# Optimization experiments

Measured on AMD Instinct MI355X. Metric: run time of the kernel, lower is better.

The kernel has to match this reference:

```python
import jax, jax.numpy as jnp
from jax import lax
import numpy as np

DIM = 192
HEADS = 8
TOPK = 2


def conv1x1(x, w):
    # x: [B,C,H,W], w: [O,C] (1x1 conv, no bias)
    return jnp.einsum('bchw,oc->bohw', x, w)


def setup_inputs() -> dict:
    key = jax.random.key(0)
    ks = jax.random.split(key, 6)
    B, C, H, W = 8, DIM, 128, 128
    x = jax.random.normal(ks[0], (B, C, H, W), jnp.float32)
    qkv_w = jax.random.normal(ks[1], (3 * C, C), jnp.float32) * 0.05
    dw_w = jax.random.normal(ks[2], (3 * C, 1, 3, 3), jnp.float32) * 0.1  # depthwise OIHW
    proj_w = jax.random.normal(ks[3], (C, C), jnp.float32) * 0.05
    router_main_w = jax.random.normal(ks[4], (HEADS, C), jnp.float32) * 0.05
    router_aux_w = jax.random.normal(ks[5], (HEADS, C), jnp.float32) * 0.05
    return dict(x=x, qkv_w=qkv_w, dw_w=dw_w, proj_w=proj_w,
                router_main_w=router_main_w, router_aux_w=router_aux_w,
                task_id=0)


def _forward(x, qkv_w, dw_w, proj_w, router_main_w, router_aux_w, task_id):
    B, C, H, W = x.shape
    heads, topk = HEADS, TOPK
    hd = C // heads
    N = H * W
    scale = hd ** -0.5

    # ---- router: softmax -> top-k -> mask -> renormalized gates ----
    rw = router_main_w if task_id == 0 else router_aux_w
    logits = jnp.einsum('bchw,oc->bohw', x, rw)                 # [B, heads, H, W]
    probs = jax.nn.softmax(
        logits.reshape(B, heads, N).transpose(0, 2, 1).reshape(B * N, heads), axis=1)
    _, idx = lax.top_k(probs, topk)                             # [B*N, topk]
    mask = lax.stop_gradient(
        jax.nn.one_hot(idx, heads, dtype=probs.dtype).sum(axis=1))  # [B*N, heads]
    masked = probs * mask
    denom = jnp.maximum(masked.sum(axis=1, keepdims=True), jnp.finfo(x.dtype).eps)
    gates = (masked / denom).reshape(B, N, heads).transpose(0, 2, 1)[:, :, None, :]  # [B, heads, 1, N]

    # ---- QKV: 1x1 conv + depthwise 3x3 conv ----
    qkv = conv1x1(x, qkv_w)                                      # [B, 3C, H, W]
    qkv = lax.conv_general_dilated(
        qkv, dw_w, window_strides=(1, 1), padding=((1, 1), (1, 1)),
        feature_group_count=3 * C,
        dimension_numbers=('NCHW', 'OIHW', 'NCHW'))
    q, k, v = jnp.split(qkv, 3, axis=1)

    def heads_view(t):  # b (h c) H W -> b h c (H W)
        return t.reshape(B, heads, hd, N)

    q, k, v = heads_view(q), heads_view(k), heads_view(v)
    # L2 normalize along the pixel axis (F.normalize, eps=1e-12)
    q = q / jnp.maximum(jnp.linalg.norm(q, axis=-1, keepdims=True), 1e-12)
    k = k / jnp.maximum(jnp.linalg.norm(k, axis=-1, keepdims=True), 1e-12)

    # channel attention: [B, heads, hd, hd] (tiny GEMM)
    attn = jax.nn.softmax(jnp.einsum('bhcn,bhdn->bhcd', q, k) * scale, axis=-1)
    out = jnp.einsum('bhcd,bhdn->bhcn', attn, v)                 # [B, heads, hd, N]

    out = out * gates * topk                                     # MoH gating
    out = out.reshape(B, C, H, W)                                # b (head c) h w
    out = conv1x1(out, proj_w)
    return out


def reference(x, qkv_w, dw_w, proj_w, router_main_w, router_aux_w, task_id):
    return _forward(x, qkv_w, dw_w, proj_w, router_main_w, router_aux_w, task_id)
```

## Files before the change

kernel.cpp:

```cpp
#include <hip/hip_runtime.h>
#include <hip/hip_bf16.h>

typedef __bf16 bf16;
typedef __bf16 bf16x8 __attribute__((ext_vector_type(8)));
typedef __bf16 bf16x4 __attribute__((ext_vector_type(4)));
typedef float f32x4 __attribute__((ext_vector_type(4)));
typedef unsigned int u32;

#define NPIX 16384
#define CDIM 192

__device__ __forceinline__ void gl2lds16(const bf16* g, const bf16* l) {
  __builtin_amdgcn_global_load_lds(
      (const __attribute__((address_space(1))) u32*)(g),
      (__attribute__((address_space(3))) u32*)(l), 16, 0, 0);
}

__global__ __launch_bounds__(256) void detect_kernel(
    const u32* __restrict__ xw, int* __restrict__ flag) {
  int tid = threadIdx.x;
  int cnt = 0;
  for (int i = 0; i < 32; i++) {
    u32 w = xw[tid * 32 + i];
    u32 e = (w >> 7) & 0xFFu;
    if (e >= 0xC0u) cnt++;
  }
  for (int off = 32; off; off >>= 1) cnt += __shfl_down(cnt, off);
  __shared__ int red[4];
  if ((tid & 63) == 0) red[tid >> 6] = cnt;
  __syncthreads();
  if (tid == 0) *flag = (red[0] + red[1] + red[2] + red[3] >= 16) ? 1 : 0;
}

__global__ __launch_bounds__(256) void wconvert_kernel(
    const void* __restrict__ s0, bf16* __restrict__ d0,
    const void* __restrict__ s1, bf16* __restrict__ d1,
    const void* __restrict__ s2, bf16* __restrict__ d2,
    const int* __restrict__ flag) {
  int which = blockIdx.y;
  const void* src = which == 0 ? s0 : (which == 1 ? s1 : s2);
  bf16* dst = which == 0 ? d0 : (which == 1 ? d1 : d2);
  int n = which == 0 ? 110592 : (which == 1 ? 5184 : 36864);
  int base = (blockIdx.x * 256 + threadIdx.x) * 8;
  if (base >= n) return;
  if (*flag) {
    const float* s = (const float*)src;
    float4 lo = *(const float4*)(s + base);
    float4 hi = *(const float4*)(s + base + 4);
    bf16x8 o;
    o[0] = (bf16)lo.x; o[1] = (bf16)lo.y; o[2] = (bf16)lo.z; o[3] = (bf16)lo.w;
    o[4] = (bf16)hi.x; o[5] = (bf16)hi.y; o[6] = (bf16)hi.z; o[7] = (bf16)hi.w;
    *(bf16x8*)(dst + base) = o;
  } else {
    *(bf16x8*)(dst + base) = *(const bf16x8*)((const bf16*)src + base);
  }
}

__global__ __launch_bounds__(256) void transpose_kernel(
    const void* __restrict__ xraw, bf16* __restrict__ xt,
    const int* __restrict__ flag, const void* __restrict__ wmain,
    const void* __restrict__ waux, const int* __restrict__ task,
    float* __restrict__ gates2) {
  __shared__ float wT[CDIM][8];
  __shared__ float lred[4][128][8];
  int t = threadIdx.x;
  int b = blockIdx.y;
  int n0 = blockIdx.x * 128;
  int f = *flag;
  const void* rw = (*task == 0) ? wmain : waux;
  for (int i = t; i < 8 * CDIM; i += 256) {
    int h = i / CDIM, c = i - h * CDIM;
    wT[c][h] = f ? ((const float*)rw)[i] : (float)((const bf16*)rw)[i];
  }
  __syncthreads();
  int nl = (t & 31) * 4;
  int cb = (t >> 5) * 8;
  float l[4][8];
#pragma unroll
  for (int j = 0; j < 4; j++)
#pragma unroll
    for (int h = 0; h < 8; h++) l[j][h] = 0.f;
  for (int ch = 0; ch < 3; ch++) {
    int c8 = ch * 64 + cb;
    float v[8][4];
    if (f) {
      const float* xp = (const float*)xraw + ((size_t)b * CDIM << 14) + n0 + nl;
#pragma unroll
      for (int i = 0; i < 8; i++) {
        float4 q = *(const float4*)(xp + ((size_t)(c8 + i) << 14));
        v[i][0] = q.x; v[i][1] = q.y; v[i][2] = q.z; v[i][3] = q.w;
      }
    } else {
      const bf16* xp = (const bf16*)xraw + ((size_t)b * CDIM << 14) + n0 + nl;
#pragma unroll
      for (int i = 0; i < 8; i++) {
        bf16x4 q = *(const bf16x4*)(xp + ((size_t)(c8 + i) << 14));
#pragma unroll
        for (int j = 0; j < 4; j++) v[i][j] = (float)q[j];
      }
    }
#pragma unroll
    for (int i = 0; i < 8; i++) {
      float4 wlo = *(const float4*)&wT[c8 + i][0];
      float4 whi = *(const float4*)&wT[c8 + i][4];
#pragma unroll
      for (int j = 0; j < 4; j++) {
        float xv = v[i][j];
        l[j][0] += xv * wlo.x; l[j][1] += xv * wlo.y;
        l[j][2] += xv * wlo.z; l[j][3] += xv * wlo.w;
        l[j][4] += xv * whi.x; l[j][5] += xv * whi.y;
        l[j][6] += xv * whi.z; l[j][7] += xv * whi.w;
      }
    }
#pragma unroll
    for (int j = 0; j < 4; j++) {
      bf16x8 o;
#pragma unroll
      for (int i = 0; i < 8; i++) o[i] = (bf16)v[i][j];
      *(bf16x8*)(xt + ((size_t)b << 14) * CDIM + (size_t)(n0 + nl + j) * CDIM + c8) = o;
    }
  }
#pragma unroll
  for (int j = 0; j < 4; j++)
#pragma unroll
    for (int h = 0; h < 8; h++) l[j][h] += __shfl_xor(l[j][h], 32);
  int lane = t & 63, wid = t >> 6;
  if (lane < 32) {
#pragma unroll
    for (int j = 0; j < 4; j++) {
      *(float4*)&lred[wid][nl + j][0] = make_float4(l[j][0], l[j][1], l[j][2], l[j][3]);
      *(float4*)&lred[wid][nl + j][4] = make_float4(l[j][4], l[j][5], l[j][6], l[j][7]);
    }
  }
  __syncthreads();
  if (t < 128) {
    float lg[8];
#pragma unroll
    for (int h = 0; h < 8; h++)
      lg[h] = (lred[0][t][h] + lred[1][t][h]) + (lred[2][t][h] + lred[3][t][h]);
    int i1 = 0;
#pragma unroll
    for (int h = 1; h < 8; h++) if (lg[h] > lg[i1]) i1 = h;
    int i2 = (i1 == 0) ? 1 : 0;
#pragma unroll
    for (int h = 0; h < 8; h++) if (h != i1 && lg[h] > lg[i2]) i2 = h;
    float e = __expf(lg[i2] - lg[i1]);
    float g1 = 2.f / (1.f + e);
    float g2 = e * g1;
    float* gb = gates2 + (((size_t)b * 8) << 14) + n0 + t;
#pragma unroll
    for (int h = 0; h < 8; h++)
      gb[(size_t)h << 14] = (h == i1) ? g1 : ((h == i2) ? g2 : 0.f);
  }
}

__global__ __launch_bounds__(256) void wgemm2_kernel(
    const bf16* __restrict__ A, const bf16* __restrict__ Xt,
    void* __restrict__ C, int M, const int* __restrict__ flag, int finalout) {
  __shared__ bf16 smem[22528];
  int tid = threadIdx.x;
  int wave = tid >> 6, lane = tid & 63;
  int c0 = lane & 15, qd = lane >> 4;

  int nm = M / 96;
  int ord = blockIdx.x + nm * (blockIdx.y + (blockIdx.z << 6));
  int z = ord & 7;
  int local = ord >> 3;
  int mt = local % nm;
  int nt = local / nm;
  int m0 = mt * 96, n0 = nt << 8;

  const bf16* Xb = Xt + (size_t)z * CDIM * NPIX;
  size_t cbase = (size_t)z * M * NPIX;

  int q = lane >> 4;
  int rr = (lane & 15) ^ (q << 1);
  const bf16* Ag0 = A + (size_t)(m0 + (wave << 4) + rr) * CDIM + (q << 3);
  const bf16* Ag1 = A + (size_t)(m0 + ((4 + wave) << 4) + rr) * CDIM + (q << 3);
  const bf16* Bg  = Xb + (size_t)(n0 + (wave << 6) + rr) * CDIM + (q << 3);

  int slot8 = ((qd << 4) + (c0 ^ (qd << 1))) << 3;

  f32x4 acc[6][4];
#pragma unroll
  for (int i = 0; i < 6; i++)
#pragma unroll
    for (int j = 0; j < 4; j++) acc[i][j] = {0.f, 0.f, 0.f, 0.f};

  auto STAGE = [&](int bb, int k) {
    gl2lds16(Ag0 + k, smem + bb + (wave << 9));
    if (wave < 2) gl2lds16(Ag1 + k, smem + bb + ((4 + wave) << 9));
    const bf16* bl = smem + bb + 3072 + (wave << 11);
    gl2lds16(Bg + k,             bl);
    gl2lds16(Bg + 16 * CDIM + k, bl + 512);
    gl2lds16(Bg + 32 * CDIM + k, bl + 1024);
    gl2lds16(Bg + 48 * CDIM + k, bl + 1536);
  };

  int bb = 0;
  STAGE(0, 0);
  __syncthreads();
  for (int t = 0; t < 6; t++) {
    if (t < 5) STAGE(bb ^ 11264, (t + 1) << 5);
    bf16x8 af[6], bfr[4];
#pragma unroll
    for (int mi = 0; mi < 6; mi++)
      af[mi] = *(const bf16x8*)(smem + bb + mi * 512 + slot8);
#pragma unroll
    for (int nj = 0; nj < 4; nj++)
      bfr[nj] = *(const bf16x8*)(smem + bb + 3072 + (wave << 11) + nj * 512 + slot8);
#pragma unroll
    for (int mi = 0; mi < 6; mi++)
#pragma unroll
      for (int nj = 0; nj < 4; nj++)
        acc[mi][nj] = __builtin_amdgcn_mfma_f32_16x16x32_bf16(bfr[nj], af[mi], acc[mi][nj], 0, 0, 0);
    if (t < 5) { __syncthreads(); bb ^= 11264; }
  }

  int f32o = finalout && (*flag);
  int n_base = n0 + (wave << 6) + (qd << 2);
#pragma unroll
  for (int mi = 0; mi < 6; mi++) {
    size_t rowb = cbase + ((size_t)(m0 + (mi << 4) + c0) << 14) + n_base;
#pragma unroll
    for (int nj = 0; nj < 4; nj++) {
      if (f32o) {
        *(float4*)((float*)C + rowb + (nj << 4)) =
            make_float4(acc[mi][nj][0], acc[mi][nj][1], acc[mi][nj][2], acc[mi][nj][3]);
      } else {
        bf16x4 o;
        o[0] = (bf16)acc[mi][nj][0]; o[1] = (bf16)acc[mi][nj][1];
        o[2] = (bf16)acc[mi][nj][2]; o[3] = (bf16)acc[mi][nj][3];
        *(bf16x4*)((bf16*)C + rowb + (nj << 4)) = o;
      }
    }
  }
}

__global__ __launch_bounds__(256) void dwconv_kernel(
    const bf16* __restrict__ qkv, const bf16* __restrict__ w9,
    bf16* __restrict__ out, float* __restrict__ sumsq) {
  int tid = threadIdx.x;
  int ch = blockIdx.y, b = blockIdx.z;
  int xs = (tid & 15) << 3;
  int y0 = (blockIdx.x << 6) + ((tid >> 4) << 2);
  const bf16* in = qkv + (((size_t)(b * 576 + ch)) << 14);
  float wv[9];
#pragma unroll
  for (int i = 0; i < 9; i++) wv[i] = (float)w9[ch * 9 + i];
  float o[4][8];
#pragma unroll
  for (int r = 0; r < 4; r++)
#pragma unroll
    for (int i = 0; i < 8; i++) o[r][i] = 0.f;
#pragma unroll
  for (int rr = 0; rr < 6; rr++) {
    int yy = y0 - 1 + rr;
    if (yy < 0 || yy > 127) continue;
    const bf16* row = in + (yy << 7);
    float vals[10];
    vals[0] = (xs > 0) ? (float)row[xs - 1] : 0.f;
    bf16x8 v8 = *(const bf16x8*)(row + xs);
#pragma unroll
    for (int j = 0; j < 8; j++) vals[1 + j] = (float)v8[j];
    vals[9] = (xs < 120) ? (float)row[xs + 8] : 0.f;
#pragma unroll
    for (int orow = 0; orow < 4; orow++) {
      int wrow = rr - orow;
      if (wrow < 0 || wrow > 2) continue;
      float w0 = wv[wrow * 3 + 0], w1 = wv[wrow * 3 + 1], w2 = wv[wrow * 3 + 2];
#pragma unroll
      for (int i = 0; i < 8; i++)
        o[orow][i] += w0 * vals[i] + w1 * vals[i + 1] + w2 * vals[i + 2];
    }
  }
  float ss = 0.f;
  bf16* ob = out + (((size_t)(b * 576 + ch)) << 14);
#pragma unroll
  for (int r = 0; r < 4; r++) {
    bf16x8 ov;
#pragma unroll
    for (int i = 0; i < 8; i++) { ov[i] = (bf16)o[r][i]; ss += o[r][i] * o[r][i]; }
    *(bf16x8*)(ob + ((y0 + r) << 7) + xs) = ov;
  }
  if (ch < 384) {
#pragma unroll
    for (int off = 32; off; off >>= 1) ss += __shfl_down(ss, off);
    __shared__ float red[4];
    if ((tid & 63) == 0) red[tid >> 6] = ss;
    __syncthreads();
    if (tid == 0) atomicAdd(&sumsq[b * 384 + ch], red[0] + red[1] + red[2] + red[3]);
  }
}

__global__ __launch_bounds__(256) void spart_kernel(
    const bf16* __restrict__ dwout, float* __restrict__ Spart) {
  int tid = threadIdx.x;
  int bh = blockIdx.y, split = blockIdx.x;
  int b = bh >> 3, h = bh & 7;
  int wave = tid >> 6, lane = tid & 63;
  int c0 = lane & 15, qd = lane >> 4;
  __shared__ float Sred[576];
  for (int i = tid; i < 576; i += 256) Sred[i] = 0.f;
  __syncthreads();
  const bf16* qb = dwout + (((size_t)(b * 576 + h * 24)) << 14);
  const bf16* kb = dwout + (((size_t)(b * 576 + 192 + h * 24)) << 14);
  int r0 = c0;
  int r1 = (16 + c0 < 24) ? (16 + c0) : 23;
  f32x4 a00 = {0.f,0.f,0.f,0.f}, a01 = {0.f,0.f,0.f,0.f};
  f32x4 a10 = {0.f,0.f,0.f,0.f}, a11 = {0.f,0.f,0.f,0.f};
  int base = (((split << 2) + wave) << 9) + (qd << 3);
  for (int t = 0; t < 16; t++) {
    int kk = base + (t << 5);
    bf16x8 qa0 = *(const bf16x8*)(qb + (((size_t)r0) << 14) + kk);
    bf16x8 qa1 = *(const bf16x8*)(qb + (((size_t)r1) << 14) + kk);
    bf16x8 ka0 = *(const bf16x8*)(kb + (((size_t)r0) << 14) + kk);
    bf16x8 ka1 = *(const bf16x8*)(kb + (((size_t)r1) << 14) + kk);
    a00 = __builtin_amdgcn_mfma_f32_16x16x32_bf16(qa0, ka0, a00, 0, 0, 0);
    a01 = __builtin_amdgcn_mfma_f32_16x16x32_bf16(qa0, ka1, a01, 0, 0, 0);
    a10 = __builtin_amdgcn_mfma_f32_16x16x32_bf16(qa1, ka0, a10, 0, 0, 0);
    a11 = __builtin_amdgcn_mfma_f32_16x16x32_bf16(qa1, ka1, a11, 0, 0, 0);
  }
  f32x4 accs[4] = {a00, a01, a10, a11};
#pragma unroll
  for (int mi = 0; mi < 2; mi++)
#pragma unroll
    for (int nj = 0; nj < 2; nj++) {
      f32x4 a = accs[mi * 2 + nj];
#pragma unroll
      for (int r = 0; r < 4; r++) {
        int rrow = (mi << 4) + (qd << 2) + r;
        int cc = (nj << 4) + c0;
        if (rrow < 24 && cc < 24) atomicAdd(&Sred[rrow * 24 + cc], a[r]);
      }
    }
  __syncthreads();
  float* outp = Spart + (size_t)(bh * 8 + split) * 576;
  for (int i = tid; i < 576; i += 256) outp[i] = Sred[i];
}

__global__ __launch_bounds__(576) void attn_kernel(
    const float* __restrict__ Spart, const float* __restrict__ sumsq,
    float* __restrict__ attn) {
  int bh = blockIdx.x, tid = threadIdx.x;
  int b = bh >> 3, h = bh & 7;
  int c = tid / 24, d = tid % 24;
  float s = 0.f;
  for (int sp = 0; sp < 8; sp++) s += Spart[(size_t)(bh * 8 + sp) * 576 + tid];
  float nq = fmaxf(sqrtf(sumsq[b * 384 + h * 24 + c]), 1e-12f);
  float nk = fmaxf(sqrtf(sumsq[b * 384 + 192 + h * 24 + d]), 1e-12f);
  s = s / (nq * nk) * 0.20412414523193154f;
  __shared__ float Sm[576];
  Sm[tid] = s;
  __syncthreads();
  float mx = -1e30f;
  for (int j = 0; j < 24; j++) mx = fmaxf(mx, Sm[c * 24 + j]);
  float Z = 0.f;
  for (int j = 0; j < 24; j++) Z += __expf(Sm[c * 24 + j] - mx);
  attn[(size_t)bh * 576 + tid] = __expf(s - mx) / Z;
}

__global__ __launch_bounds__(256) void av_kernel(
    const bf16* __restrict__ dwout, const float* __restrict__ attn,
    const float* __restrict__ gates2, bf16* __restrict__ gated_t) {
  int tid = threadIdx.x;
  int bh = blockIdx.y;
  int b = bh >> 3, h = bh & 7;
  int n = blockIdx.x * 256 + tid;
  __shared__ float At[576];
  for (int i = tid; i < 576; i += 256) At[i] = attn[(size_t)bh * 576 + i];
  __syncthreads();
  const bf16* vb = dwout + (((size_t)(b * 576 + 384 + h * 24)) << 14) + n;
  float acc[24];
#pragma unroll
  for (int c = 0; c < 24; c++) acc[c] = 0.f;
#pragma unroll
  for (int d0 = 0; d0 < 24; d0 += 4) {
    float v0 = (float)vb[(size_t)(d0 + 0) << 14];
    float v1 = (float)vb[(size_t)(d0 + 1) << 14];
    float v2 = (float)vb[(size_t)(d0 + 2) << 14];
    float v3 = (float)vb[(size_t)(d0 + 3) << 14];
#pragma unroll
    for (int c = 0; c < 24; c++) {
      const float4* ap = (const float4*)&At[c * 24 + d0];
      acc[c] += ap->x * v0 + ap->y * v1 + ap->z * v2 + ap->w * v3;
    }
  }
  float g = gates2[(((size_t)(b * 8 + h)) << 14) + n];
  bf16* ob = gated_t + ((size_t)(b * NPIX + n)) * CDIM + h * 24;
#pragma unroll
  for (int ch = 0; ch < 3; ch++) {
    bf16x8 o;
#pragma unroll
    for (int i = 0; i < 8; i++) o[i] = (bf16)(acc[ch * 8 + i] * g);
    *(bf16x8*)(ob + ch * 8) = o;
  }
}

extern "C" void kernel_launch(void* const* d_in, const int* in_sizes, int n_in,
                              void* d_out, int out_size, void* d_ws, size_t ws_size,
                              hipStream_t stream) {
  const void* x_raw    = d_in[0];
  const void* qkvw_raw = d_in[1];
  const void* dww_raw  = d_in[2];
  const void* projw_raw= d_in[3];
  const void* rtm_raw  = d_in[4];
  const void* rta_raw  = d_in[5];
  const int*  task     = (const int*)d_in[6];
  char* ws = (char*)d_ws;

  bf16*  qkv_raw = (bf16*)(ws);
  bf16*  gated_t = qkv_raw;
  bf16*  dwout   = (bf16*)(ws + 150994944);
  float* gates2  = (float*)(ws + 301989888);
  float* sumsq   = (float*)(ws + 306184192);
  float* Spart   = (float*)(ws + 306196480);
  float* attn    = (float*)(ws + 307376128);
  int*   flag    = (int*)(ws + 307523584);
  bf16*  xt      = (bf16*)(ws + 307523712);
  bf16*  qkv_wb  = (bf16*)(ws + 357855360);
  bf16*  dw_wb   = (bf16*)(ws + 358076544);
  bf16*  proj_wb = (bf16*)(ws + 358086912);

  hipMemsetAsync(sumsq, 0, 8 * 384 * sizeof(float), stream);
  detect_kernel<<<1, 256, 0, stream>>>((const u32*)x_raw, flag);
  wconvert_kernel<<<dim3(54, 3), 256, 0, stream>>>(qkvw_raw, qkv_wb, dww_raw, dw_wb,
                                                   projw_raw, proj_wb, flag);
  transpose_kernel<<<dim3(128, 8), 256, 0, stream>>>(x_raw, xt, flag,
                                                     rtm_raw, rta_raw, task, gates2);
  wgemm2_kernel<<<dim3(6, 64, 8), 256, 0, stream>>>(qkv_wb, xt, qkv_raw, 576, flag, 0);
  dwconv_kernel<<<dim3(2, 576, 8), 256, 0, stream>>>(qkv_raw, dw_wb, dwout, sumsq);
  spart_kernel<<<dim3(8, 64), 256, 0, stream>>>(dwout, Spart);
  attn_kernel<<<64, 576, 0, stream>>>(Spart, sumsq, attn);
  av_kernel<<<dim3(64, 64), 256, 0, stream>>>(dwout, attn, gates2, gated_t);
  wgemm2_kernel<<<dim3(2, 64, 8), 256, 0, stream>>>(proj_wb, gated_t, d_out, 192, flag, 1);
}
```

Before: 448.5 us.

## Load GEMM operands directly from global memory instead of staging through LDS

The weight GEMM kernel drops its double-buffered global-to-LDS staging and the barriers between K steps. Each wave now reads its MFMA fragments for A and B straight from global memory in a fully unrolled K loop. This removes LDS traffic and block-wide synchronisation, and the compiler can schedule all the loads early. In exchange every wave re-reads the shared A tile from global or L2, and the per-lane 16-byte loads with a row stride of CDIM may coalesce less well.

```diff
diff --git a/kernel.cpp b/kernel.cpp
--- a/kernel.cpp
+++ b/kernel.cpp
@@ -9,12 +9,6 @@
 
 #define NPIX 16384
 #define CDIM 192
-
-__device__ __forceinline__ void gl2lds16(const bf16* g, const bf16* l) {
-  __builtin_amdgcn_global_load_lds(
-      (const __attribute__((address_space(1))) u32*)(g),
-      (__attribute__((address_space(3))) u32*)(l), 16, 0, 0);
-}
 
 __global__ __launch_bounds__(256) void detect_kernel(
     const u32* __restrict__ xw, int* __restrict__ flag) {
@@ -157,7 +151,6 @@
 __global__ __launch_bounds__(256) void wgemm2_kernel(
     const bf16* __restrict__ A, const bf16* __restrict__ Xt,
     void* __restrict__ C, int M, const int* __restrict__ flag, int finalout) {
-  __shared__ bf16 smem[22528];
   int tid = threadIdx.x;
   int wave = tid >> 6, lane = tid & 63;
   int c0 = lane & 15, qd = lane >> 4;
@@ -173,13 +166,8 @@
   const bf16* Xb = Xt + (size_t)z * CDIM * NPIX;
   size_t cbase = (size_t)z * M * NPIX;
 
-  int q = lane >> 4;
-  int rr = (lane & 15) ^ (q << 1);
-  const bf16* Ag0 = A + (size_t)(m0 + (wave << 4) + rr) * CDIM + (q << 3);
-  const bf16* Ag1 = A + (size_t)(m0 + ((4 + wave) << 4) + rr) * CDIM + (q << 3);
-  const bf16* Bg  = Xb + (size_t)(n0 + (wave << 6) + rr) * CDIM + (q << 3);
-
-  int slot8 = ((qd << 4) + (c0 ^ (qd << 1))) << 3;
+  const bf16* Ap = A + (size_t)(m0 + c0) * CDIM + (qd << 3);
+  const bf16* Bp = Xb + (size_t)(n0 + (wave << 6) + c0) * CDIM + (qd << 3);
 
   f32x4 acc[6][4];
 #pragma unroll
@@ -187,34 +175,20 @@
 #pragma unroll
     for (int j = 0; j < 4; j++) acc[i][j] = {0.f, 0.f, 0.f, 0.f};
 
-  auto STAGE = [&](int bb, int k) {
-    gl2lds16(Ag0 + k, smem + bb + (wave << 9));
-    if (wave < 2) gl2lds16(Ag1 + k, smem + bb + ((4 + wave) << 9));
-    const bf16* bl = smem + bb + 3072 + (wave << 11);
-    gl2lds16(Bg + k,             bl);
-    gl2lds16(Bg + 16 * CDIM + k, bl + 512);
-    gl2lds16(Bg + 32 * CDIM + k, bl + 1024);
-    gl2lds16(Bg + 48 * CDIM + k, bl + 1536);
-  };
-
-  int bb = 0;
-  STAGE(0, 0);
-  __syncthreads();
-  for (int t = 0; t < 6; t++) {
-    if (t < 5) STAGE(bb ^ 11264, (t + 1) << 5);
+#pragma unroll
+  for (int k0 = 0; k0 < CDIM; k0 += 32) {
     bf16x8 af[6], bfr[4];
 #pragma unroll
+    for (int nj = 0; nj < 4; nj++)
+      bfr[nj] = *(const bf16x8*)(Bp + (size_t)(nj << 4) * CDIM + k0);
+#pragma unroll
     for (int mi = 0; mi < 6; mi++)
-      af[mi] = *(const bf16x8*)(smem + bb + mi * 512 + slot8);
-#pragma unroll
-    for (int nj = 0; nj < 4; nj++)
-      bfr[nj] = *(const bf16x8*)(smem + bb + 3072 + (wave << 11) + nj * 512 + slot8);
+      af[mi] = *(const bf16x8*)(Ap + (size_t)(mi << 4) * CDIM + k0);
 #pragma unroll
     for (int mi = 0; mi < 6; mi++)
 #pragma unroll
       for (int nj = 0; nj < 4; nj++)
         acc[mi][nj] = __builtin_amdgcn_mfma_f32_16x16x32_bf16(bfr[nj], af[mi], acc[mi][nj], 0, 0, 0);
-    if (t < 5) { __syncthreads(); bb ^= 11264; }
   }
 
   int f32o = finalout && (*flag);
```

Result: slower. 481.8 us (+7.4%).

## Pre-swizzle GEMM operands into tile-contiguous blocked layout for LDS loads

Applied to the files above, without the earlier changes.

The producers (weight conversion, input transpose, gated attention output) now write GEMM operands in a blocked K-chunk-major layout that already carries the LDS swizzle. The GEMM staging then reads contiguous 1KB chunks per wave instead of row-strided 16-byte pieces, which should give better-coalesced global-to-LDS transfers. The cost is more complex index math in the producer stores, and every consumer of these buffers must agree on the new layout.

```diff
diff --git a/kernel.cpp b/kernel.cpp
--- a/kernel.cpp
+++ b/kernel.cpp
@@ -9,6 +9,7 @@
 
 #define NPIX 16384
 #define CDIM 192
+
 
 __device__ __forceinline__ void gl2lds16(const bf16* g, const bf16* l) {
   __builtin_amdgcn_global_load_lds(
@@ -43,16 +44,25 @@
   int n = which == 0 ? 110592 : (which == 1 ? 5184 : 36864);
   int base = (blockIdx.x * 256 + threadIdx.x) * 8;
   if (base >= n) return;
+  bf16x8 o;
   if (*flag) {
     const float* s = (const float*)src;
     float4 lo = *(const float4*)(s + base);
     float4 hi = *(const float4*)(s + base + 4);
-    bf16x8 o;
     o[0] = (bf16)lo.x; o[1] = (bf16)lo.y; o[2] = (bf16)lo.z; o[3] = (bf16)lo.w;
     o[4] = (bf16)hi.x; o[5] = (bf16)hi.y; o[6] = (bf16)hi.z; o[7] = (bf16)hi.w;
+  } else {
+    o = *(const bf16x8*)((const bf16*)src + base);
+  }
+  if (which != 1) {
+    int M = (which == 0) ? 576 : 192;
+    int m = base / 192, k = base - m * 192;
+    int kc = k >> 5, j8 = (k >> 3) & 3;
+    size_t dstoff = (size_t)kc * M * 32 + ((size_t)(m >> 4) << 9)
+                  + (((j8 << 4) + ((m & 15) ^ (j8 << 1))) << 3);
+    *(bf16x8*)(dst + dstoff) = o;
+  } else {
     *(bf16x8*)(dst + base) = o;
-  } else {
-    *(bf16x8*)(dst + base) = *(const bf16x8*)((const bf16*)src + base);
   }
 }
 
@@ -112,12 +122,17 @@
         l[j][6] += xv * whi.z; l[j][7] += xv * whi.w;
       }
     }
+    int kc = c8 >> 5, j8 = (c8 >> 3) & 3;
+    size_t pb = (((size_t)b * 6 + kc) << 19);
 #pragma unroll
     for (int j = 0; j < 4; j++) {
       bf16x8 o;
 #pragma unroll
       for (int i = 0; i < 8; i++) o[i] = (bf16)v[i][j];
-      *(bf16x8*)(xt + ((size_t)b << 14) * CDIM + (size_t)(n0 + nl + j) * CDIM + c8) = o;
+      int nn = n0 + nl + j;
+      size_t dst = pb + ((size_t)(nn >> 4) << 9)
+                 + (((j8 << 4) + ((nn & 15) ^ (j8 << 1))) << 3);
+      *(bf16x8*)(xt + dst) = o;
     }
   }
 #pragma unroll
@@ -172,12 +187,7 @@
 
   const bf16* Xb = Xt + (size_t)z * CDIM * NPIX;
   size_t cbase = (size_t)z * M * NPIX;
-
-  int q = lane >> 4;
-  int rr = (lane & 15) ^ (q << 1);
-  const bf16* Ag0 = A + (size_t)(m0 + (wave << 4) + rr) * CDIM + (q << 3);
-  const bf16* Ag1 = A + (size_t)(m0 + ((4 + wave) << 4) + rr) * CDIM + (q << 3);
-  const bf16* Bg  = Xb + (size_t)(n0 + (wave << 6) + rr) * CDIM + (q << 3);
+  int Mx32 = M * 32;
 
   int slot8 = ((qd << 4) + (c0 ^ (qd << 1))) << 3;
 
@@ -187,21 +197,24 @@
 #pragma unroll
     for (int j = 0; j < 4; j++) acc[i][j] = {0.f, 0.f, 0.f, 0.f};
 
-  auto STAGE = [&](int bb, int k) {
-    gl2lds16(Ag0 + k, smem + bb + (wave << 9));
-    if (wave < 2) gl2lds16(Ag1 + k, smem + bb + ((4 + wave) << 9));
+  auto STAGE = [&](int bb, int kc) {
+    const bf16* As = A + (size_t)kc * Mx32 + mt * 3072 + (lane << 3);
+    const bf16* Bs = Xb + ((size_t)kc << 19)
+                   + ((size_t)((nt << 4) + (wave << 2)) << 9) + (lane << 3);
+    gl2lds16(As + (wave << 9), smem + bb + (wave << 9));
+    if (wave < 2) gl2lds16(As + ((4 + wave) << 9), smem + bb + ((4 + wave) << 9));
     const bf16* bl = smem + bb + 3072 + (wave << 11);
-    gl2lds16(Bg + k,             bl);
-    gl2lds16(Bg + 16 * CDIM + k, bl + 512);
-    gl2lds16(Bg + 32 * CDIM + k, bl + 1024);
-    gl2lds16(Bg + 48 * CDIM + k, bl + 1536);
+    gl2lds16(Bs,        bl);
+    gl2lds16(Bs +  512, bl + 512);
+    gl2lds16(Bs + 1024, bl + 1024);
+    gl2lds16(Bs + 1536, bl + 1536);
   };
 
   int bb = 0;
   STAGE(0, 0);
   __syncthreads();
   for (int t = 0; t < 6; t++) {
-    if (t < 5) STAGE(bb ^ 11264, (t + 1) << 5);
+    if (t < 5) STAGE(bb ^ 11264, t + 1);
     bf16x8 af[6], bfr[4];
 #pragma unroll
     for (int mi = 0; mi < 6; mi++)
@@ -387,13 +400,16 @@
     }
   }
   float g = gates2[(((size_t)(b * 8 + h)) << 14) + n];
-  bf16* ob = gated_t + ((size_t)(b * NPIX + n)) * CDIM + h * 24;
 #pragma unroll
   for (int ch = 0; ch < 3; ch++) {
     bf16x8 o;
 #pragma unroll
     for (int i = 0; i < 8; i++) o[i] = (bf16)(acc[ch * 8 + i] * g);
-    *(bf16x8*)(ob + ch * 8) = o;
+    int c = h * 24 + ch * 8;
+    int kc = c >> 5, j8 = (c >> 3) & 3;
+    size_t dst = (((size_t)b * 6 + kc) << 19) + ((size_t)(n >> 4) << 9)
+               + (((j8 << 4) + ((n & 15) ^ (j8 << 1))) << 3);
+    *(bf16x8*)(gated_t + dst) = o;
   }
 }
 
```

New measurement: 425.9 us. 5.0% less time.
